# Kernel tuning notes

Hardware: AMD Instinct MI355X
Metric: run time of the kernel (lower is better)

Reference implementation:

```python
import jax, jax.numpy as jnp
import numpy as np

EPS = 1e-6
N_HEADS = 128
QK_NOPE = 128
QK_ROPE = 64
KV_RANK = 512

def rmsnorm(x, gamma):
    var = jnp.mean(jnp.square(x), axis=-1, keepdims=True)
    return x * jax.lax.rsqrt(var + EPS) * gamma

def apply_rope(x, cos, sin):
    # x: [..., D], cos/sin broadcastable to x; rotate-half convention
    x1, x2 = jnp.split(x, 2, axis=-1)
    rot = jnp.concatenate([-x2, x1], axis=-1)
    return x * cos + rot * sin

def setup_inputs() -> dict:
    key = jax.random.key(0)
    ks = jax.random.split(key, 6)
    T, H = 4096, 7168
    inp = {
        "token_x": jax.random.normal(ks[0], (T, H), jnp.float32),
        "wq_a": jax.random.normal(ks[1], (H, 1536), jnp.float32) * 0.02,
        "wq_b": jax.random.normal(ks[2], (1536, N_HEADS * (QK_NOPE + QK_ROPE)), jnp.float32) * 0.02,
        "wkv": jax.random.normal(ks[3], (H, KV_RANK + QK_ROPE), jnp.float32) * 0.02,
        "rope_cos": jax.random.uniform(ks[4], (T, QK_ROPE), jnp.float32, -1.0, 1.0),
        "rope_sin": jax.random.uniform(ks[5], (T, QK_ROPE), jnp.float32, -1.0, 1.0),
        "gamma_cq": jnp.ones((1536,), jnp.float32),
        "gamma_ckv": jnp.ones((KV_RANK,), jnp.float32),
    }
    return inp

def reference(token_x, wq_a, wq_b, wkv, rope_cos, rope_sin, gamma_cq, gamma_ckv):
    T = token_x.shape[0]
    # Query path: down-proj -> RMSNorm -> up-proj -> split -> RoPE on rope part
    cq = rmsnorm(token_x @ wq_a, gamma_cq)                    # [T, 1536]
    q = (cq @ wq_b).reshape(T, N_HEADS, QK_NOPE + QK_ROPE)    # [T, H, 192]
    q_nope, q_rope = q[..., :QK_NOPE], q[..., QK_NOPE:]
    q_rope = apply_rope(q_rope, rope_cos[:, None, :], rope_sin[:, None, :])
    query = jnp.concatenate([q_nope, q_rope], axis=-1)        # [T, H, 192]
    # KV path: joint down-proj -> split latent / rope-key -> RMSNorm + RoPE
    kv = token_x @ wkv                                        # [T, 576]
    ckv = rmsnorm(kv[:, :KV_RANK], gamma_ckv)                 # [T, 512]
    k_rope = apply_rope(kv[:, KV_RANK:], rope_cos, rope_sin)  # [T, 64]
    # Pack outputs into a single array: [T, H*192 + 512 + 64]
    return jnp.concatenate([query.reshape(T, -1), ckv, k_rope], axis=-1)
```

## Files before the change

### kernel.cpp

```cpp
#include <hip/hip_runtime.h>


typedef __attribute__((ext_vector_type(8))) __bf16 bf16x8;
typedef __attribute__((ext_vector_type(4))) float f32x4;

#define OUT_LD 25152

__device__ __forceinline__ unsigned short f2bf(float f) {
  union { float f; unsigned u; } v; v.f = f;
  unsigned r = v.u + 0x7FFFu + ((v.u >> 16) & 1u);
  return (unsigned short)(r >> 16);
}

__device__ __forceinline__ void gload16(const void* g, void* l) {
  __builtin_amdgcn_global_load_lds(
      (__attribute__((address_space(1))) void*)(void*)g,
      (__attribute__((address_space(3))) void*)l, 16, 0, 0);
}

__global__ void cvt_bf16(const float* __restrict__ in, unsigned short* __restrict__ out) {
  size_t i = (size_t)blockIdx.x * 256 + threadIdx.x;
  float4 f = ((const float4*)in)[i];
  ushort4 o;
  o.x = f2bf(f.x); o.y = f2bf(f.y); o.z = f2bf(f.z); o.w = f2bf(f.w);
  ((ushort4*)out)[i] = o;
}

__global__ void transpose_cvt(const float* __restrict__ in, unsigned short* __restrict__ out,
                              int K, int N, int Npad) {
  __shared__ float tile[32][33];
  int k0 = blockIdx.x * 32, n0 = blockIdx.y * 32;
  int tx = threadIdx.x, ty = threadIdx.y;
#pragma unroll
  for (int i = 0; i < 4; ++i) {
    int k = k0 + ty + i * 8;
    int n = n0 + tx;
    tile[ty + i * 8][tx] = (n < N) ? in[(size_t)k * N + n] : 0.f;
  }
  __syncthreads();
#pragma unroll
  for (int i = 0; i < 4; ++i) {
    int n = n0 + ty + i * 8;
    int k = k0 + tx;
    if (n < Npad) out[(size_t)n * K + k] = f2bf(tile[tx][ty + i * 8]);
  }
}

__global__ __launch_bounds__(512, 2) void gemm256(
    const unsigned short* __restrict__ A, const unsigned short* __restrict__ B,
    float* __restrict__ C, int K, int ldc, int Mtiles,
    const float* __restrict__ cs, const float* __restrict__ sn, int rope) {
  __shared__ __attribute__((aligned(128))) char lds[131072];
  const int tid = threadIdx.x;
  const int lane = tid & 63;
  const int wr = (tid >> 6) >> 2;
  const int wc = (tid >> 6) & 3;
  const int NT = K >> 6;

  const int nwg = gridDim.x;
  const int per = nwg >> 3;
  const int bid = blockIdx.x;
  const int swz = (bid & 7) * per + (bid >> 3);
  const int bm = swz % Mtiles, bn = swz / Mtiles;

  const int strow = tid >> 3;
  const int stcolb = (((tid & 7) ^ ((tid >> 3) & 7)) << 4);
  const size_t abase = (size_t)(bm * 256) * K;
  const size_t bbase = (size_t)(bn * 256) * K;

  f32x4 acc[2][2][4][2];
  const f32x4 z4 = {0.f, 0.f, 0.f, 0.f};
#pragma unroll
  for (int a = 0; a < 2; ++a)
#pragma unroll
    for (int b = 0; b < 2; ++b)
#pragma unroll
      for (int c = 0; c < 4; ++c)
#pragma unroll
        for (int d = 0; d < 2; ++d) acc[a][b][c][d] = z4;

#define STAGE_A(kt, bsel, u)                                                          \
  do {                                                                                \
    int row_ = (u) * 64 + strow;                                                      \
    gload16((const char*)(A + abase + (size_t)row_ * K + (size_t)(kt) * 64) + stcolb, \
            lds + (bsel) * 65536 + (u) * 8192 + tid * 16);                            \
  } while (0)
#define STAGE_B(kt, bsel, u)                                                          \
  do {                                                                                \
    int lrow_ = (u) * 64 + strow;                                                     \
    int n_ = ((lrow_ >> 5) & 3) * 64 + ((lrow_ >> 7) & 1) * 32 + (lrow_ & 31);        \
    gload16((const char*)(B + bbase + (size_t)n_ * K + (size_t)(kt) * 64) + stcolb,   \
            lds + (bsel) * 65536 + 32768 + (u) * 8192 + tid * 16);                    \
  } while (0)

#define READ_A(dst, QM, LBASE)                                              \
  do {                                                                      \
    _Pragma("unroll") for (int mf = 0; mf < 4; ++mf)                        \
        _Pragma("unroll") for (int ks = 0; ks < 2; ++ks) {                  \
      int row_ = (QM) * 128 + wr * 64 + mf * 16 + (lane & 15);              \
      int in_ = (ks * 64 + ((lane >> 4) << 4)) ^ ((row_ & 7) << 4);         \
      dst[mf][ks] = *(const bf16x8*)((LBASE) + row_ * 128 + in_);           \
    }                                                                       \
  } while (0)
#define READ_B(dst, QN, LBASE)                                              \
  do {                                                                      \
    _Pragma("unroll") for (int nf = 0; nf < 2; ++nf)                        \
        _Pragma("unroll") for (int ks = 0; ks < 2; ++ks) {                  \
      int c_ = wc * 64 + (QN) * 32 + nf * 16 + (lane & 15);                 \
      int rr_ = ((c_ >> 5) & 1) * 128 + ((c_ >> 6) & 3) * 32 + (c_ & 31);   \
      int in_ = (ks * 64 + ((lane >> 4) << 4)) ^ ((rr_ & 7) << 4);          \
      dst[nf][ks] = *(const bf16x8*)((LBASE) + 32768 + rr_ * 128 + in_);    \
    }                                                                       \
  } while (0)
#define MFMA_Q(QM, QN, AF, BB)                                              \
  do {                                                                      \
    _Pragma("unroll") for (int mf = 0; mf < 4; ++mf)                        \
        _Pragma("unroll") for (int nf = 0; nf < 2; ++nf)                    \
            _Pragma("unroll") for (int ks = 0; ks < 2; ++ks)                \
                acc[QM][QN][mf][nf] = __builtin_amdgcn_mfma_f32_16x16x32_bf16( \
                    AF[mf][ks], BB[nf][ks], acc[QM][QN][mf][nf], 0, 0, 0);  \
  } while (0)

  STAGE_A(0, 0, 0); STAGE_A(0, 0, 1); STAGE_A(0, 0, 2); STAGE_A(0, 0, 3);
  STAGE_B(0, 0, 0); STAGE_B(0, 0, 1); STAGE_B(0, 0, 2); STAGE_B(0, 0, 3);
  __syncthreads();

  bf16x8 af0[4][2], af1[4][2], bb0[2][2], bb1[2][2];

  for (int t = 0; t < NT; ++t) {
    const int buf = t & 1;
    const int pb = buf ^ 1;
    const char* Lb = lds + buf * 65536;

    if (t + 1 < NT) {
      STAGE_A(t + 1, pb, 0); STAGE_A(t + 1, pb, 1);
      STAGE_A(t + 1, pb, 2); STAGE_A(t + 1, pb, 3);
      STAGE_B(t + 1, pb, 0); STAGE_B(t + 1, pb, 1);
      STAGE_B(t + 1, pb, 2); STAGE_B(t + 1, pb, 3);
    }

    READ_A(af0, 0, Lb);
    READ_B(bb0, 0, Lb);
    READ_B(bb1, 1, Lb);
    READ_A(af1, 1, Lb);

    __builtin_amdgcn_s_setprio(1);
    MFMA_Q(0, 0, af0, bb0);
    MFMA_Q(0, 1, af0, bb1);
    MFMA_Q(1, 1, af1, bb1);
    MFMA_Q(1, 0, af1, bb0);
    __builtin_amdgcn_s_setprio(0);

    __syncthreads();
  }

  const int colbase = bn * 256 + wc * 64;
  const int rbase = bm * 256 + wr * 64 + ((lane >> 4) << 2);
  const bool isrope = rope && ((colbase % 192) == 128);
  if (isrope) {
#pragma unroll
    for (int qm = 0; qm < 2; ++qm)
#pragma unroll
      for (int mf = 0; mf < 4; ++mf)
#pragma unroll
        for (int nf = 0; nf < 2; ++nf) {
          int i_ = nf * 16 + (lane & 15);
#pragma unroll
          for (int r = 0; r < 4; ++r) {
            int trow = rbase + qm * 128 + mf * 16 + r;
            float c1 = cs[trow * 64 + i_], s1 = sn[trow * 64 + i_];
            float c2 = cs[trow * 64 + 32 + i_], s2 = sn[trow * 64 + 32 + i_];
            float a = acc[qm][0][mf][nf][r], b = acc[qm][1][mf][nf][r];
            C[(size_t)trow * ldc + colbase + i_] = a * c1 - b * s1;
            C[(size_t)trow * ldc + colbase + 32 + i_] = b * c2 + a * s2;
          }
        }
  } else {
#pragma unroll
    for (int qm = 0; qm < 2; ++qm)
#pragma unroll
      for (int qn = 0; qn < 2; ++qn)
#pragma unroll
        for (int mf = 0; mf < 4; ++mf)
#pragma unroll
          for (int nf = 0; nf < 2; ++nf)
#pragma unroll
            for (int r = 0; r < 4; ++r) {
              int trow = rbase + qm * 128 + mf * 16 + r;
              C[(size_t)trow * ldc + colbase + qn * 32 + nf * 16 + (lane & 15)] =
                  acc[qm][qn][mf][nf][r];
            }
  }
#undef MFMA_Q
#undef READ_B
#undef READ_A
#undef STAGE_B
#undef STAGE_A
}

__global__ __launch_bounds__(256, 2) void gemm128(
    const unsigned short* __restrict__ A, const unsigned short* __restrict__ B,
    float* __restrict__ C, int K, int ldc, int Nvalid) {
  __shared__ __attribute__((aligned(128))) unsigned short As[128 * 32];
  __shared__ __attribute__((aligned(128))) unsigned short Bs[128 * 32];
  const int tid = threadIdx.x;
  const int lane = tid & 63;
  const int wid = tid >> 6;
  const int wr = wid >> 1, wc = wid & 1;
  const int bm = blockIdx.y, bn = blockIdx.x;
  const size_t abase = (size_t)bm * 128 * K;
  const size_t bbase = (size_t)bn * 128 * K;

  f32x4 acc[4][4];
  const f32x4 zero4 = {0.f, 0.f, 0.f, 0.f};
#pragma unroll
  for (int m = 0; m < 4; ++m)
#pragma unroll
    for (int n = 0; n < 4; ++n) acc[m][n] = zero4;

  const int r0 = tid >> 2;
  const int c0 = (tid & 3) * 8;

  for (int k0 = 0; k0 < K; k0 += 32) {
    gload16(A + abase + (size_t)r0 * K + k0 + c0, As + tid * 8);
    gload16(A + abase + (size_t)(r0 + 64) * K + k0 + c0, As + (256 + tid) * 8);
    gload16(B + bbase + (size_t)r0 * K + k0 + c0, Bs + tid * 8);
    gload16(B + bbase + (size_t)(r0 + 64) * K + k0 + c0, Bs + (256 + tid) * 8);
    __syncthreads();
    bf16x8 af[4], bfr[4];
#pragma unroll
    for (int m = 0; m < 4; ++m)
      af[m] = *(const bf16x8*)(As + (wr * 64 + m * 16 + (lane & 15)) * 32 + (lane >> 4) * 8);
#pragma unroll
    for (int n = 0; n < 4; ++n)
      bfr[n] = *(const bf16x8*)(Bs + (wc * 64 + n * 16 + (lane & 15)) * 32 + (lane >> 4) * 8);
#pragma unroll
    for (int m = 0; m < 4; ++m)
#pragma unroll
      for (int n = 0; n < 4; ++n)
        acc[m][n] = __builtin_amdgcn_mfma_f32_16x16x32_bf16(af[m], bfr[n], acc[m][n], 0, 0, 0);
    __syncthreads();
  }

  const int crow0 = bm * 128 + wr * 64 + ((lane >> 4) << 2);
  const int ccol0 = bn * 128 + wc * 64 + (lane & 15);
#pragma unroll
  for (int m = 0; m < 4; ++m) {
#pragma unroll
    for (int n = 0; n < 4; ++n) {
      int col = ccol0 + n * 16;
      if (col < Nvalid) {
#pragma unroll
        for (int r = 0; r < 4; ++r) {
          int row = crow0 + m * 16 + r;
          C[(size_t)row * ldc + col] = acc[m][n][r];
        }
      }
    }
  }
}

__global__ void epi1(const float* __restrict__ raw, const float* __restrict__ gcq,
                     const float* __restrict__ gckv, const float* __restrict__ cs,
                     const float* __restrict__ sn, unsigned short* __restrict__ cqb,
                     float* __restrict__ out) {
  __shared__ float red[4];
  int t = blockIdx.x, tid = threadIdx.x;
  const float* r = raw + (size_t)t * 2176;
  float v[6];
  float ss = 0.f;
#pragma unroll
  for (int i = 0; i < 6; ++i) {
    v[i] = r[tid + i * 256];
    ss += v[i] * v[i];
  }
#pragma unroll
  for (int o = 32; o > 0; o >>= 1) ss += __shfl_xor(ss, o, 64);
  if ((tid & 63) == 0) red[tid >> 6] = ss;
  __syncthreads();
  ss = red[0] + red[1] + red[2] + red[3];
  float sc = rsqrtf(ss * (1.f / 1536.f) + 1e-6f);
#pragma unroll
  for (int i = 0; i < 6; ++i)
    cqb[(size_t)t * 1536 + tid + i * 256] = f2bf(v[i] * sc * gcq[tid + i * 256]);
  float v0 = r[1536 + tid], v1 = r[1792 + tid];
  float s2 = v0 * v0 + v1 * v1;
#pragma unroll
  for (int o = 32; o > 0; o >>= 1) s2 += __shfl_xor(s2, o, 64);
  __syncthreads();
  if ((tid & 63) == 0) red[tid >> 6] = s2;
  __syncthreads();
  s2 = red[0] + red[1] + red[2] + red[3];
  float sck = rsqrtf(s2 * (1.f / 512.f) + 1e-6f);
  float* orow = out + (size_t)t * OUT_LD + 24576;
  orow[tid] = v0 * sck * gckv[tid];
  orow[tid + 256] = v1 * sck * gckv[tid + 256];
  if (tid < 32) {
    float a = r[2048 + tid], b = r[2080 + tid];
    orow[512 + tid] = a * cs[t * 64 + tid] - b * sn[t * 64 + tid];
    orow[544 + tid] = b * cs[t * 64 + 32 + tid] + a * sn[t * 64 + 32 + tid];
  }
}

extern "C" void kernel_launch(void* const* d_in, const int* in_sizes, int n_in,
                              void* d_out, int out_size, void* d_ws, size_t ws_size,
                              hipStream_t stream) {
  const float* token_x = (const float*)d_in[0];
  const float* wq_a = (const float*)d_in[1];
  const float* wq_b = (const float*)d_in[2];
  const float* wkv = (const float*)d_in[3];
  const float* rope_cos = (const float*)d_in[4];
  const float* rope_sin = (const float*)d_in[5];
  const float* gamma_cq = (const float*)d_in[6];
  const float* gamma_ckv = (const float*)d_in[7];
  float* out = (float*)d_out;

  char* ws = (char*)d_ws;
  unsigned short* txb = (unsigned short*)ws;
  unsigned short* wqbT = (unsigned short*)(ws + 58720256);
  unsigned short* Bc = (unsigned short*)(ws + 134217728);
  float* raw = (float*)(ws + 165412864);
  unsigned short* cqb = (unsigned short*)(ws + 201064448);

  cvt_bf16<<<28672, 256, 0, stream>>>(token_x, txb);
  transpose_cvt<<<dim3(7168 / 32, 1536 / 32), dim3(32, 8), 0, stream>>>(wq_a, Bc, 7168, 1536, 1536);
  transpose_cvt<<<dim3(7168 / 32, 640 / 32), dim3(32, 8), 0, stream>>>(
      wkv, Bc + (size_t)1536 * 7168, 7168, 576, 640);
  transpose_cvt<<<dim3(1536 / 32, 24576 / 32), dim3(32, 8), 0, stream>>>(wq_b, wqbT, 1536, 24576, 24576);

  gemm128<<<dim3(17, 32), 256, 0, stream>>>(txb, Bc, raw, 7168, 2176, 2176);

  epi1<<<4096, 256, 0, stream>>>(raw, gamma_cq, gamma_ckv, rope_cos, rope_sin, cqb, out);

  gemm256<<<1536, 512, 0, stream>>>(cqb, wqbT, out, 1536, OUT_LD, 16, rope_cos, rope_sin, 1);
}
```

Baseline: 684.1 us.

## Interleave LDS reads, global prefetch and MFMA phases with explicit barriers

Restructures the 256x256 GEMM main loop into four phases, each separated by s_barrier and explicit lgkmcnt/vmcnt waits. LDS fragment reads and the next tile's global-to-LDS staging are spread across the MFMA quadrants instead of being issued all at once. The aim is to overlap memory traffic with matrix math and keep waves in lockstep, a ping-pong style schedule. The cost is several extra workgroup barriers per iteration and manual waitcnt handling, which could stall waves or be unsafe if the counts are wrong.

```diff
diff --git a/kernel.cpp b/kernel.cpp
--- a/kernel.cpp
+++ b/kernel.cpp
@@ -121,9 +121,16 @@
                     AF[mf][ks], BB[nf][ks], acc[QM][QN][mf][nf], 0, 0, 0);  \
   } while (0)
 
+#define LGKM0_FENCE()                                  \
+  do {                                                 \
+    asm volatile("s_waitcnt lgkmcnt(0)" ::: "memory"); \
+    __builtin_amdgcn_sched_barrier(0);                 \
+  } while (0)
+
   STAGE_A(0, 0, 0); STAGE_A(0, 0, 1); STAGE_A(0, 0, 2); STAGE_A(0, 0, 3);
   STAGE_B(0, 0, 0); STAGE_B(0, 0, 1); STAGE_B(0, 0, 2); STAGE_B(0, 0, 3);
-  __syncthreads();
+  asm volatile("s_waitcnt vmcnt(0)" ::: "memory");
+  __builtin_amdgcn_s_barrier();
 
   bf16x8 af0[4][2], af1[4][2], bb0[2][2], bb1[2][2];
 
@@ -132,26 +139,45 @@
     const int pb = buf ^ 1;
     const char* Lb = lds + buf * 65536;
 
+    READ_A(af0, 0, Lb);
+    READ_B(bb0, 0, Lb);
     if (t + 1 < NT) {
       STAGE_A(t + 1, pb, 0); STAGE_A(t + 1, pb, 1);
       STAGE_A(t + 1, pb, 2); STAGE_A(t + 1, pb, 3);
+    }
+    __builtin_amdgcn_s_barrier();
+    LGKM0_FENCE();
+    __builtin_amdgcn_s_setprio(1);
+    MFMA_Q(0, 0, af0, bb0);
+    __builtin_amdgcn_s_setprio(0);
+    __builtin_amdgcn_s_barrier();
+
+    READ_B(bb1, 1, Lb);
+    if (t + 1 < NT) {
       STAGE_B(t + 1, pb, 0); STAGE_B(t + 1, pb, 1);
       STAGE_B(t + 1, pb, 2); STAGE_B(t + 1, pb, 3);
     }
-
-    READ_A(af0, 0, Lb);
-    READ_B(bb0, 0, Lb);
-    READ_B(bb1, 1, Lb);
+    __builtin_amdgcn_s_barrier();
+    LGKM0_FENCE();
+    __builtin_amdgcn_s_setprio(1);
+    MFMA_Q(0, 1, af0, bb1);
+    __builtin_amdgcn_s_setprio(0);
+    __builtin_amdgcn_s_barrier();
+
     READ_A(af1, 1, Lb);
-
+    __builtin_amdgcn_s_barrier();
+    LGKM0_FENCE();
     __builtin_amdgcn_s_setprio(1);
-    MFMA_Q(0, 0, af0, bb0);
-    MFMA_Q(0, 1, af0, bb1);
     MFMA_Q(1, 1, af1, bb1);
+    __builtin_amdgcn_s_setprio(0);
+    __builtin_amdgcn_s_barrier();
+
+    __builtin_amdgcn_s_setprio(1);
     MFMA_Q(1, 0, af1, bb0);
     __builtin_amdgcn_s_setprio(0);
-
-    __syncthreads();
+    asm volatile("s_waitcnt vmcnt(0)" ::: "memory");
+    __builtin_amdgcn_s_barrier();
+    __builtin_amdgcn_sched_barrier(0);
   }
 
   const int colbase = bn * 256 + wc * 64;
@@ -191,6 +217,7 @@
                   acc[qm][qn][mf][nf][r];
             }
   }
+#undef LGKM0_FENCE
 #undef MFMA_Q
 #undef READ_B
 #undef READ_A
```

New measurement: 699.0 us. 2.2% more time.

## Double-buffer gemm128 and add fine-grained waitcnt scheduling to main GEMM loop

Applied to the files above, without the earlier changes.

The main 256x256 GEMM loop now uses explicit vmcnt/lgkmcnt waits and sched_barriers in place of __syncthreads. MFMA groups can start once only their operand LDS reads have landed, and each group gets its own priority bump. The smaller gemm128 kernel switches from a single LDS buffer to double buffering, prefetching the next K-tile while computing the current one. This is meant to overlap global loads and LDS reads with MFMA work. It doubles gemm128's LDS use and relies on hand-counted lgkmcnt values being correct.

```diff
diff --git a/kernel.cpp b/kernel.cpp
--- a/kernel.cpp
+++ b/kernel.cpp
@@ -114,16 +114,20 @@
   } while (0)
 #define MFMA_Q(QM, QN, AF, BB)                                              \
   do {                                                                      \
+    __builtin_amdgcn_s_setprio(1);                                          \
     _Pragma("unroll") for (int mf = 0; mf < 4; ++mf)                        \
         _Pragma("unroll") for (int nf = 0; nf < 2; ++nf)                    \
             _Pragma("unroll") for (int ks = 0; ks < 2; ++ks)                \
                 acc[QM][QN][mf][nf] = __builtin_amdgcn_mfma_f32_16x16x32_bf16( \
                     AF[mf][ks], BB[nf][ks], acc[QM][QN][mf][nf], 0, 0, 0);  \
+    __builtin_amdgcn_s_setprio(0);                                          \
   } while (0)
 
   STAGE_A(0, 0, 0); STAGE_A(0, 0, 1); STAGE_A(0, 0, 2); STAGE_A(0, 0, 3);
   STAGE_B(0, 0, 0); STAGE_B(0, 0, 1); STAGE_B(0, 0, 2); STAGE_B(0, 0, 3);
-  __syncthreads();
+  asm volatile("s_waitcnt vmcnt(0)" ::: "memory");
+  __builtin_amdgcn_s_barrier();
+  __builtin_amdgcn_sched_barrier(0);
 
   bf16x8 af0[4][2], af1[4][2], bb0[2][2], bb1[2][2];
 
@@ -138,20 +142,32 @@
       STAGE_B(t + 1, pb, 0); STAGE_B(t + 1, pb, 1);
       STAGE_B(t + 1, pb, 2); STAGE_B(t + 1, pb, 3);
     }
+    __builtin_amdgcn_sched_barrier(0);
 
     READ_A(af0, 0, Lb);
     READ_B(bb0, 0, Lb);
+    __builtin_amdgcn_sched_barrier(0);
     READ_B(bb1, 1, Lb);
+    __builtin_amdgcn_sched_barrier(0);
     READ_A(af1, 1, Lb);
-
-    __builtin_amdgcn_s_setprio(1);
+    __builtin_amdgcn_sched_barrier(0);
+
+    asm volatile("s_waitcnt lgkmcnt(12)" ::: "memory");
+    __builtin_amdgcn_sched_barrier(0);
     MFMA_Q(0, 0, af0, bb0);
+
+    asm volatile("s_waitcnt lgkmcnt(8)" ::: "memory");
+    __builtin_amdgcn_sched_barrier(0);
     MFMA_Q(0, 1, af0, bb1);
+
+    asm volatile("s_waitcnt lgkmcnt(0)" ::: "memory");
+    __builtin_amdgcn_sched_barrier(0);
     MFMA_Q(1, 1, af1, bb1);
     MFMA_Q(1, 0, af1, bb0);
-    __builtin_amdgcn_s_setprio(0);
-
-    __syncthreads();
+
+    asm volatile("s_waitcnt vmcnt(0)" ::: "memory");
+    __builtin_amdgcn_s_barrier();
+    __builtin_amdgcn_sched_barrier(0);
   }
 
   const int colbase = bn * 256 + wc * 64;
@@ -201,8 +217,8 @@
 __global__ __launch_bounds__(256, 2) void gemm128(
     const unsigned short* __restrict__ A, const unsigned short* __restrict__ B,
     float* __restrict__ C, int K, int ldc, int Nvalid) {
-  __shared__ __attribute__((aligned(128))) unsigned short As[128 * 32];
-  __shared__ __attribute__((aligned(128))) unsigned short Bs[128 * 32];
+  __shared__ __attribute__((aligned(128))) unsigned short As[2][128 * 32];
+  __shared__ __attribute__((aligned(128))) unsigned short Bs[2][128 * 32];
   const int tid = threadIdx.x;
   const int lane = tid & 63;
   const int wid = tid >> 6;
@@ -220,27 +236,47 @@
 
   const int r0 = tid >> 2;
   const int c0 = (tid & 3) * 8;
-
-  for (int k0 = 0; k0 < K; k0 += 32) {
-    gload16(A + abase + (size_t)r0 * K + k0 + c0, As + tid * 8);
-    gload16(A + abase + (size_t)(r0 + 64) * K + k0 + c0, As + (256 + tid) * 8);
-    gload16(B + bbase + (size_t)r0 * K + k0 + c0, Bs + tid * 8);
-    gload16(B + bbase + (size_t)(r0 + 64) * K + k0 + c0, Bs + (256 + tid) * 8);
-    __syncthreads();
+  const int NT = K >> 5;
+
+#define G128_STAGE(kt, bsel)                                                   \
+  do {                                                                         \
+    gload16(A + abase + (size_t)r0 * K + (kt) * 32 + c0, As[bsel] + tid * 8);  \
+    gload16(A + abase + (size_t)(r0 + 64) * K + (kt) * 32 + c0,                \
+            As[bsel] + (256 + tid) * 8);                                       \
+    gload16(B + bbase + (size_t)r0 * K + (kt) * 32 + c0, Bs[bsel] + tid * 8);  \
+    gload16(B + bbase + (size_t)(r0 + 64) * K + (kt) * 32 + c0,                \
+            Bs[bsel] + (256 + tid) * 8);                                       \
+  } while (0)
+
+  G128_STAGE(0, 0);
+  __syncthreads();
+
+  for (int t = 0; t < NT; ++t) {
+    const int buf = t & 1;
+    const int pb = buf ^ 1;
+    if (t + 1 < NT) G128_STAGE(t + 1, pb);
+
     bf16x8 af[4], bfr[4];
 #pragma unroll
     for (int m = 0; m < 4; ++m)
-      af[m] = *(const bf16x8*)(As + (wr * 64 + m * 16 + (lane & 15)) * 32 + (lane >> 4) * 8);
+      af[m] = *(const bf16x8*)(As[buf] + (wr * 64 + m * 16 + (lane & 15)) * 32 + (lane >> 4) * 8);
 #pragma unroll
     for (int n = 0; n < 4; ++n)
-      bfr[n] = *(const bf16x8*)(Bs + (wc * 64 + n * 16 + (lane & 15)) * 32 + (lane >> 4) * 8);
+      bfr[n] = *(const bf16x8*)(Bs[buf] + (wc * 64 + n * 16 + (lane & 15)) * 32 + (lane >> 4) * 8);
+
+    asm volatile("s_waitcnt lgkmcnt(0)" ::: "memory");
+    __builtin_amdgcn_sched_barrier(0);
+    __builtin_amdgcn_s_setprio(1);
 #pragma unroll
     for (int m = 0; m < 4; ++m)
 #pragma unroll
       for (int n = 0; n < 4; ++n)
         acc[m][n] = __builtin_amdgcn_mfma_f32_16x16x32_bf16(af[m], bfr[n], acc[m][n], 0, 0, 0);
+    __builtin_amdgcn_s_setprio(0);
+
     __syncthreads();
   }
+#undef G128_STAGE
 
   const int crow0 = bm * 128 + wr * 64 + ((lane >> 4) << 2);
   const int ccol0 = bn * 128 + wc * 64 + (lane & 15);
```

Result: no change. 684.8 us (median of 3 runs) (+0.1%).
